# Performance work log

Measured on AMD Instinct MI355X. Metric: run time of the kernel, lower is better.

The kernel has to match this reference:

```python
import jax, jax.numpy as jnp
import numpy as np

B, N, C_IN, C_MID, H, N_CLS = 128, 2048, 3, 64, 128, 40
EPS = 1e-5

def setup_inputs() -> dict:
    key = jax.random.key(0)
    ks = jax.random.split(key, 12)
    sc = lambda fan: 1.0 / np.sqrt(fan)
    return {
        "x": jax.random.normal(ks[0], (B, N, C_IN), jnp.float32),
        "conv_w": jax.random.normal(ks[1], (C_MID, C_IN), jnp.float32) * sc(C_IN),
        "conv_b": jnp.zeros((C_MID,), jnp.float32),
        "gamma": jnp.ones((C_MID,), jnp.float32),
        "beta": jnp.zeros((C_MID,), jnp.float32),
        "running_mean": jax.random.normal(ks[2], (C_MID,), jnp.float32) * 0.1,
        "running_var": jax.random.uniform(ks[3], (C_MID,), jnp.float32) + 0.5,
        "W_ih": jax.random.normal(ks[4], (4 * H, C_MID), jnp.float32) * sc(H),
        "W_hh": jax.random.normal(ks[5], (4 * H, H), jnp.float32) * sc(H),
        "b_ih": jax.random.normal(ks[6], (4 * H,), jnp.float32) * sc(H),
        "b_hh": jax.random.normal(ks[7], (4 * H,), jnp.float32) * sc(H),
        "W_out": jax.random.normal(ks[8], (N_CLS, H), jnp.float32) * sc(H),
        "b_out": jnp.zeros((N_CLS,), jnp.float32),
    }

def reference(x, conv_w, conv_b, gamma, beta, running_mean, running_var,
              W_ih, W_hh, b_ih, b_hh, W_out, b_out):
    # Conv1d(3,64,1) == per-point linear; BN (inference form) + ReLU.  [B,N,64]
    h = jnp.einsum('bnc,oc->bno', x, conv_w) + conv_b
    inv = gamma * jax.lax.rsqrt(running_var + EPS)
    h = jax.nn.relu((h - running_mean) * inv + beta)
    # Precompute input-side gate projections for all timesteps: [B,N,4H]
    xg = jnp.einsum('bnc,gc->bng', h, W_ih) + b_ih + b_hh
    Whh_T = W_hh.T  # [H,4H]

    def step(carry, xg_t):
        h_prev, c_prev = carry
        g = xg_t + h_prev @ Whh_T  # [B,4H]
        i, f, gg, o = jnp.split(g, 4, axis=-1)  # PyTorch gate order i,f,g,o
        i = jax.nn.sigmoid(i)
        f = jax.nn.sigmoid(f)
        gg = jnp.tanh(gg)
        o = jax.nn.sigmoid(o)
        c = f * c_prev + i * gg
        h_new = o * jnp.tanh(c)
        return (h_new, c), None

    init = (jnp.zeros((x.shape[0], W_hh.shape[1]), x.dtype),
            jnp.zeros((x.shape[0], W_hh.shape[1]), x.dtype))
    (h_last, _), _ = jax.lax.scan(step, init, jnp.swapaxes(xg, 0, 1))
    # Only the last timestep feeds the classifier head.
    return h_last @ W_out.T + b_out
```

## Files before the change

### kernel.cpp

```cpp
#include <hip/hip_runtime.h>
#include <math.h>

#define BB 128
#define NN 2048
#define CMID 64
#define HH 128
#define NCLS 40
#define CHUNK 128
#define EPSV 1e-5f

#define HCP 80
#define HP  36

__device__ __forceinline__ float fsigmoid(float x) {
    return 1.0f / (1.0f + __expf(-x));
}
__device__ __forceinline__ float ftanh2(float x) {
    return 2.0f / (1.0f + __expf(-2.0f * x)) - 1.0f;
}
__device__ __forceinline__ void fma4(float& a, const float4 w, const float4 v) {
    a = fmaf(w.x, v.x, a);
    a = fmaf(w.y, v.y, a);
    a = fmaf(w.z, v.z, a);
    a = fmaf(w.w, v.w, a);
}

__global__ __attribute__((amdgpu_flat_work_group_size(512, 512),
                          amdgpu_waves_per_eu(2, 2)))
void lstm_seq_kernel(const float* __restrict__ x,
                     const float* __restrict__ conv_w, const float* __restrict__ conv_b,
                     const float* __restrict__ gamma,  const float* __restrict__ beta,
                     const float* __restrict__ rmean,  const float* __restrict__ rvar,
                     const float* __restrict__ W_ih,   const float* __restrict__ W_hh,
                     const float* __restrict__ b_ih,   const float* __restrict__ b_hh,
                     const float* __restrict__ W_out,  const float* __restrict__ b_out,
                     float* __restrict__ out)
{
    __shared__ float hc_s[CHUNK * HCP];
    __shared__ float h_s[2][4 * HP];
    __shared__ float cA0[CMID], cA1[CMID], cA2[CMID], cD[CMID];

    const int t = threadIdx.x;
    const int b = blockIdx.x;
    const int j = t >> 2;
    const int s = t & 3;

    if (t < CMID) {
        float inv = gamma[t] * rsqrtf(rvar[t] + EPSV);
        cA0[t] = conv_w[t * 3 + 0] * inv;
        cA1[t] = conv_w[t * 3 + 1] * inv;
        cA2[t] = conv_w[t * 3 + 2] * inv;
        cD[t]  = (conv_b[t] - rmean[t]) * inv + beta[t];
    }
    if (t < 2 * 4 * HP) ((float*)h_s)[t] = 0.0f;

    float4 wih[4][4];
    float4 whh[4][8];
    float  bias[4];
    #pragma unroll
    for (int g = 0; g < 4; ++g) {
        const int r = g * HH + j;
        const float* pih = W_ih + (size_t)r * CMID + s * 16;
        #pragma unroll
        for (int i = 0; i < 4; ++i) wih[g][i] = *(const float4*)(pih + 4 * i);
        const float* phh = W_hh + (size_t)r * HH + s * 32;
        #pragma unroll
        for (int i = 0; i < 8; ++i) whh[g][i] = *(const float4*)(phh + 4 * i);
        bias[g] = b_ih[r] + b_hh[r];
    }

    float c_reg = 0.0f;
    const float* xb = x + (size_t)b * NN * 3;

    for (int ch = 0; ch < NN / CHUNK; ++ch) {
        const int base = ch * CHUNK;
        __syncthreads();

        #pragma unroll
        for (int i = 0; i < (CHUNK * CMID) / 512; ++i) {
            int v  = i * 512 + t;
            int n  = v >> 6;
            int cc = v & 63;
            float x0 = xb[(base + n) * 3 + 0];
            float x1 = xb[(base + n) * 3 + 1];
            float x2 = xb[(base + n) * 3 + 2];
            float hcv = fmaxf(cD[cc] + cA0[cc] * x0 + cA1[cc] * x1 + cA2[cc] * x2, 0.0f);
            hc_s[n * HCP + (cc >> 4) * 20 + (cc & 15)] = hcv;
        }
        __syncthreads();

        for (int k = 0; k < CHUNK; ++k) {
            const int p = (base + k) & 1;
            float a0 = 0.f, a1 = 0.f, a2 = 0.f, a3 = 0.f;

            const float4* hcp = (const float4*)&hc_s[k * HCP + s * 20];
            const float4* hp  = (const float4*)&h_s[p][s * HP];

            #pragma unroll
            for (int i = 0; i < 4; ++i) {
                float4 v = hcp[i];
                fma4(a0, wih[0][i], v); fma4(a1, wih[1][i], v);
                fma4(a2, wih[2][i], v); fma4(a3, wih[3][i], v);
            }
            #pragma unroll
            for (int i = 0; i < 8; ++i) {
                float4 u = hp[i];
                fma4(a0, whh[0][i], u); fma4(a1, whh[1][i], u);
                fma4(a2, whh[2][i], u); fma4(a3, whh[3][i], u);
            }

            #pragma unroll
            for (int m = 1; m <= 2; m <<= 1) {
                a0 += __shfl_xor(a0, m);
                a1 += __shfl_xor(a1, m);
                a2 += __shfl_xor(a2, m);
                a3 += __shfl_xor(a3, m);
            }

            float gi = fsigmoid(a0 + bias[0]);
            float gf = fsigmoid(a1 + bias[1]);
            float gg = ftanh2(a2 + bias[2]);
            float go = fsigmoid(a3 + bias[3]);
            c_reg = gf * c_reg + gi * gg;
            float hv = go * ftanh2(c_reg);

            if (s == 0) h_s[p ^ 1][(j >> 5) * HP + (j & 31)] = hv;
            __syncthreads();
        }
    }

    if (t < NCLS) {
        float acc = b_out[t];
        const float* wr = W_out + (size_t)t * HH;
        #pragma unroll
        for (int jj = 0; jj < HH; ++jj)
            acc = fmaf(wr[jj], h_s[0][(jj >> 5) * HP + (jj & 31)], acc);
        out[(size_t)b * NCLS + t] = acc;
    }
}

extern "C" void kernel_launch(void* const* d_in, const int* in_sizes, int n_in,
                              void* d_out, int out_size, void* d_ws, size_t ws_size,
                              hipStream_t stream) {
    const float* x      = (const float*)d_in[0];
    const float* conv_w = (const float*)d_in[1];
    const float* conv_b = (const float*)d_in[2];
    const float* gamma  = (const float*)d_in[3];
    const float* beta   = (const float*)d_in[4];
    const float* rmean  = (const float*)d_in[5];
    const float* rvar   = (const float*)d_in[6];
    const float* W_ih   = (const float*)d_in[7];
    const float* W_hh   = (const float*)d_in[8];
    const float* b_ih   = (const float*)d_in[9];
    const float* b_hh   = (const float*)d_in[10];
    const float* W_out  = (const float*)d_in[11];
    const float* b_out  = (const float*)d_in[12];
    float* out = (float*)d_out;

    lstm_seq_kernel<<<BB, 512, 0, stream>>>(x, conv_w, conv_b, gamma, beta,
                                            rmean, rvar, W_ih, W_hh, b_ih, b_hh,
                                            W_out, b_out, out);
}
```

Before: 1.927 ms.

## Split each LSTM row pair across 8 lanes with reshaped shared-memory layouts

Changes the work split so each group of 8 lanes handles two hidden units (j and j+64) over 8-wide input slices, in place of one unit over 4-wide slices. Shared buffers are relaid out (unpadded hc_s, h_p[2][8][20]), the reduction uses three shuffle stages, and weight preloads go through inline-asm loads that wait after each one. The aim is to reduce shared-memory read traffic per lane and give more independent FMA chains per step. In exchange the timestep loop carries more shuffles and duplicated activation math, and the unpadded hc_s layout may cause bank conflicts.

```diff
diff --git a/kernel.cpp b/kernel.cpp
--- a/kernel.cpp
+++ b/kernel.cpp
@@ -8,9 +8,6 @@
 #define NCLS 40
 #define CHUNK 128
 #define EPSV 1e-5f
-
-#define HCP 80
-#define HP  36
 
 __device__ __forceinline__ float fsigmoid(float x) {
     return 1.0f / (1.0f + __expf(-x));
@@ -24,6 +21,18 @@
     a = fmaf(w.z, v.z, a);
     a = fmaf(w.w, v.w, a);
 }
+__device__ __forceinline__ float4 pin_load4(const float* p) {
+    float4 r;
+    asm volatile("global_load_dwordx4 %0, %1, off\n\ts_waitcnt vmcnt(0)"
+                 : "=v"(r) : "v"(p) : "memory");
+    return r;
+}
+__device__ __forceinline__ float pin_load1(const float* p) {
+    float r;
+    asm volatile("global_load_dword %0, %1, off\n\ts_waitcnt vmcnt(0)"
+                 : "=v"(r) : "v"(p) : "memory");
+    return r;
+}
 
 __global__ __attribute__((amdgpu_flat_work_group_size(512, 512),
                           amdgpu_waves_per_eu(2, 2)))
@@ -36,14 +45,14 @@
                      const float* __restrict__ W_out,  const float* __restrict__ b_out,
                      float* __restrict__ out)
 {
-    __shared__ float hc_s[CHUNK * HCP];
-    __shared__ float h_s[2][4 * HP];
+    __shared__ float hc_s[CHUNK * CMID];
+    __shared__ float h_p[2][8][20];
     __shared__ float cA0[CMID], cA1[CMID], cA2[CMID], cD[CMID];
 
     const int t = threadIdx.x;
     const int b = blockIdx.x;
-    const int j = t >> 2;
-    const int s = t & 3;
+    const int g = t >> 3;
+    const int s = t & 7;
 
     if (t < CMID) {
         float inv = gamma[t] * rsqrtf(rvar[t] + EPSV);
@@ -52,24 +61,27 @@
         cA2[t] = conv_w[t * 3 + 2] * inv;
         cD[t]  = (conv_b[t] - rmean[t]) * inv + beta[t];
     }
-    if (t < 2 * 4 * HP) ((float*)h_s)[t] = 0.0f;
+    if (t < 2 * 8 * 20) ((float*)h_p)[t] = 0.0f;
 
-    float4 wih[4][4];
-    float4 whh[4][8];
-    float  bias[4];
+    float4 wih[4][2][2];
+    float4 whh[4][2][4];
+    float  bias[4][2];
     #pragma unroll
-    for (int g = 0; g < 4; ++g) {
-        const int r = g * HH + j;
-        const float* pih = W_ih + (size_t)r * CMID + s * 16;
+    for (int q = 0; q < 4; ++q) {
         #pragma unroll
-        for (int i = 0; i < 4; ++i) wih[g][i] = *(const float4*)(pih + 4 * i);
-        const float* phh = W_hh + (size_t)r * HH + s * 32;
-        #pragma unroll
-        for (int i = 0; i < 8; ++i) whh[g][i] = *(const float4*)(phh + 4 * i);
-        bias[g] = b_ih[r] + b_hh[r];
+        for (int u = 0; u < 2; ++u) {
+            const int r = q * HH + g + u * 64;
+            const float* pih = W_ih + (size_t)r * CMID + s * 8;
+            wih[q][u][0] = pin_load4(pih);
+            wih[q][u][1] = pin_load4(pih + 4);
+            const float* phh = W_hh + (size_t)r * HH + s * 16;
+            #pragma unroll
+            for (int i = 0; i < 4; ++i) whh[q][u][i] = pin_load4(phh + 4 * i);
+            bias[q][u] = pin_load1(b_ih + r) + pin_load1(b_hh + r);
+        }
     }
 
-    float c_reg = 0.0f;
+    float c0 = 0.0f, c1 = 0.0f;
     const float* xb = x + (size_t)b * NN * 3;
 
     for (int ch = 0; ch < NN / CHUNK; ++ch) {
@@ -85,46 +97,62 @@
             float x1 = xb[(base + n) * 3 + 1];
             float x2 = xb[(base + n) * 3 + 2];
             float hcv = fmaxf(cD[cc] + cA0[cc] * x0 + cA1[cc] * x1 + cA2[cc] * x2, 0.0f);
-            hc_s[n * HCP + (cc >> 4) * 20 + (cc & 15)] = hcv;
+            hc_s[n * CMID + cc] = hcv;
         }
         __syncthreads();
 
+        #pragma unroll 2
         for (int k = 0; k < CHUNK; ++k) {
-            const int p = (base + k) & 1;
-            float a0 = 0.f, a1 = 0.f, a2 = 0.f, a3 = 0.f;
+            const int p = k & 1;
+            float a[4][2] = {{0.f, 0.f}, {0.f, 0.f}, {0.f, 0.f}, {0.f, 0.f}};
 
-            const float4* hcp = (const float4*)&hc_s[k * HCP + s * 20];
-            const float4* hp  = (const float4*)&h_s[p][s * HP];
+            const float4* hcp = (const float4*)&hc_s[k * CMID + s * 8];
+            const float4* hp  = (const float4*)&h_p[p][s][0];
 
+            float4 v0 = hcp[0], v1 = hcp[1];
+            #pragma unroll
+            for (int q = 0; q < 4; ++q) {
+                fma4(a[q][0], wih[q][0][0], v0); fma4(a[q][1], wih[q][1][0], v0);
+                fma4(a[q][0], wih[q][0][1], v1); fma4(a[q][1], wih[q][1][1], v1);
+            }
             #pragma unroll
             for (int i = 0; i < 4; ++i) {
-                float4 v = hcp[i];
-                fma4(a0, wih[0][i], v); fma4(a1, wih[1][i], v);
-                fma4(a2, wih[2][i], v); fma4(a3, wih[3][i], v);
-            }
-            #pragma unroll
-            for (int i = 0; i < 8; ++i) {
-                float4 u = hp[i];
-                fma4(a0, whh[0][i], u); fma4(a1, whh[1][i], u);
-                fma4(a2, whh[2][i], u); fma4(a3, whh[3][i], u);
+                float4 uv = hp[i];
+                #pragma unroll
+                for (int q = 0; q < 4; ++q) {
+                    fma4(a[q][0], whh[q][0][i], uv);
+                    fma4(a[q][1], whh[q][1][i], uv);
+                }
             }
 
             #pragma unroll
-            for (int m = 1; m <= 2; m <<= 1) {
-                a0 += __shfl_xor(a0, m);
-                a1 += __shfl_xor(a1, m);
-                a2 += __shfl_xor(a2, m);
-                a3 += __shfl_xor(a3, m);
+            for (int m = 1; m <= 4; m <<= 1) {
+                #pragma unroll
+                for (int q = 0; q < 4; ++q) {
+                    a[q][0] += __shfl_xor(a[q][0], m);
+                    a[q][1] += __shfl_xor(a[q][1], m);
+                }
             }
 
-            float gi = fsigmoid(a0 + bias[0]);
-            float gf = fsigmoid(a1 + bias[1]);
-            float gg = ftanh2(a2 + bias[2]);
-            float go = fsigmoid(a3 + bias[3]);
-            c_reg = gf * c_reg + gi * gg;
-            float hv = go * ftanh2(c_reg);
+            float gi0 = fsigmoid(a[0][0] + bias[0][0]);
+            float gf0 = fsigmoid(a[1][0] + bias[1][0]);
+            float gg0 = ftanh2 (a[2][0] + bias[2][0]);
+            float go0 = fsigmoid(a[3][0] + bias[3][0]);
+            float gi1 = fsigmoid(a[0][1] + bias[0][1]);
+            float gf1 = fsigmoid(a[1][1] + bias[1][1]);
+            float gg1 = ftanh2 (a[2][1] + bias[2][1]);
+            float go1 = fsigmoid(a[3][1] + bias[3][1]);
 
-            if (s == 0) h_s[p ^ 1][(j >> 5) * HP + (j & 31)] = hv;
+            c0 = gf0 * c0 + gi0 * gg0;
+            c1 = gf1 * c1 + gi1 * gg1;
+            float hv0 = go0 * ftanh2(c0);
+            float hv1 = go1 * ftanh2(c1);
+
+            if (s == 0) {
+                const int j1 = g + 64;
+                h_p[p ^ 1][g >> 4][g & 15]   = hv0;
+                h_p[p ^ 1][j1 >> 4][j1 & 15] = hv1;
+            }
             __syncthreads();
         }
     }
@@ -134,7 +162,7 @@
         const float* wr = W_out + (size_t)t * HH;
         #pragma unroll
         for (int jj = 0; jj < HH; ++jj)
-            acc = fmaf(wr[jj], h_s[0][(jj >> 5) * HP + (jj & 31)], acc);
+            acc = fmaf(wr[jj], h_p[0][jj >> 4][jj & 15], acc);
         out[(size_t)b * NCLS + t] = acc;
     }
 }
```

After: 3.058 ms. 1.59x slower.

## Precompute input gate projections per chunk into LDS before the recurrent loop

Applied to the files above, without the earlier changes.

Each chunk's input-side gate projections (W_ih times conv features plus bias) are now computed as a register-tiled batched matmul into shared memory. This takes the W_ih multiply off the serial per-timestep critical path, so each step only does the W_hh matvec plus a read of the precomputed gates. It also frees the W_ih registers and changes the launch bounds. In exchange, W_ih is reloaded from global/L2 for every chunk, the chunk size is halved, and more LDS is used.

```diff
diff --git a/kernel.cpp b/kernel.cpp
--- a/kernel.cpp
+++ b/kernel.cpp
@@ -5,12 +5,11 @@
 #define NN 2048
 #define CMID 64
 #define HH 128
+#define G4 512
 #define NCLS 40
-#define CHUNK 128
+#define CH 64
+#define NCH (NN / CH)
 #define EPSV 1e-5f
-
-#define HCP 80
-#define HP  36
 
 __device__ __forceinline__ float fsigmoid(float x) {
     return 1.0f / (1.0f + __expf(-x));
@@ -25,8 +24,7 @@
     a = fmaf(w.w, v.w, a);
 }
 
-__global__ __attribute__((amdgpu_flat_work_group_size(512, 512),
-                          amdgpu_waves_per_eu(2, 2)))
+__global__ __launch_bounds__(512, 1)
 void lstm_seq_kernel(const float* __restrict__ x,
                      const float* __restrict__ conv_w, const float* __restrict__ conv_b,
                      const float* __restrict__ gamma,  const float* __restrict__ beta,
@@ -36,9 +34,11 @@
                      const float* __restrict__ W_out,  const float* __restrict__ b_out,
                      float* __restrict__ out)
 {
-    __shared__ float hc_s[CHUNK * HCP];
-    __shared__ float h_s[2][4 * HP];
-    __shared__ float cA0[CMID], cA1[CMID], cA2[CMID], cD[CMID];
+    __shared__ float xg_s[CH][G4];
+    __shared__ float hcT[CMID][CH];
+    __shared__ float h_p[2][4][36];
+    __shared__ float bias_s[G4];
+    __shared__ float cf[4][CMID];
 
     const int t = threadIdx.x;
     const int b = blockIdx.x;
@@ -47,84 +47,119 @@
 
     if (t < CMID) {
         float inv = gamma[t] * rsqrtf(rvar[t] + EPSV);
-        cA0[t] = conv_w[t * 3 + 0] * inv;
-        cA1[t] = conv_w[t * 3 + 1] * inv;
-        cA2[t] = conv_w[t * 3 + 2] * inv;
-        cD[t]  = (conv_b[t] - rmean[t]) * inv + beta[t];
+        cf[0][t] = conv_w[t * 3 + 0] * inv;
+        cf[1][t] = conv_w[t * 3 + 1] * inv;
+        cf[2][t] = conv_w[t * 3 + 2] * inv;
+        cf[3][t] = (conv_b[t] - rmean[t]) * inv + beta[t];
     }
-    if (t < 2 * 4 * HP) ((float*)h_s)[t] = 0.0f;
+    bias_s[t] = b_ih[t] + b_hh[t];
+    if (t < 2 * 4 * 36) ((float*)h_p)[t] = 0.0f;
 
-    float4 wih[4][4];
     float4 whh[4][8];
-    float  bias[4];
     #pragma unroll
-    for (int g = 0; g < 4; ++g) {
-        const int r = g * HH + j;
-        const float* pih = W_ih + (size_t)r * CMID + s * 16;
+    for (int q = 0; q < 4; ++q) {
+        const float* p = W_hh + (size_t)(q * HH + j) * HH + s * 32;
         #pragma unroll
-        for (int i = 0; i < 4; ++i) wih[g][i] = *(const float4*)(pih + 4 * i);
-        const float* phh = W_hh + (size_t)r * HH + s * 32;
-        #pragma unroll
-        for (int i = 0; i < 8; ++i) whh[g][i] = *(const float4*)(phh + 4 * i);
-        bias[g] = b_ih[r] + b_hh[r];
+        for (int i = 0; i < 8; ++i) whh[q][i] = *(const float4*)(p + 4 * i);
     }
 
     float c_reg = 0.0f;
     const float* xb = x + (size_t)b * NN * 3;
 
-    for (int ch = 0; ch < NN / CHUNK; ++ch) {
-        const int base = ch * CHUNK;
+    for (int ch = 0; ch < NCH; ++ch) {
+        const int base = ch * CH;
         __syncthreads();
 
-        #pragma unroll
-        for (int i = 0; i < (CHUNK * CMID) / 512; ++i) {
-            int v  = i * 512 + t;
-            int n  = v >> 6;
-            int cc = v & 63;
+        {
+            const int n = t & 63;
+            const int c0 = t >> 6;
             float x0 = xb[(base + n) * 3 + 0];
             float x1 = xb[(base + n) * 3 + 1];
             float x2 = xb[(base + n) * 3 + 2];
-            float hcv = fmaxf(cD[cc] + cA0[cc] * x0 + cA1[cc] * x1 + cA2[cc] * x2, 0.0f);
-            hc_s[n * HCP + (cc >> 4) * 20 + (cc & 15)] = hcv;
+            #pragma unroll
+            for (int i = 0; i < 8; ++i) {
+                int c = i * 8 + c0;
+                float hv = cf[3][c] + cf[0][c] * x0 + cf[1][c] * x1 + cf[2][c] * x2;
+                hcT[c][n] = fmaxf(hv, 0.0f);
+            }
         }
         __syncthreads();
 
-        for (int k = 0; k < CHUNK; ++k) {
-            const int p = (base + k) & 1;
-            float a0 = 0.f, a1 = 0.f, a2 = 0.f, a3 = 0.f;
-
-            const float4* hcp = (const float4*)&hc_s[k * HCP + s * 20];
-            const float4* hp  = (const float4*)&h_s[p][s * HP];
-
+        for (int pass = 0; pass < 2; ++pass) {
+            const int r0 = (pass * 2 + 0) * HH + j;
+            const int r1 = (pass * 2 + 1) * HH + j;
+            float acc0[16], acc1[16];
+            const float b0 = bias_s[r0], b1 = bias_s[r1];
             #pragma unroll
-            for (int i = 0; i < 4; ++i) {
-                float4 v = hcp[i];
-                fma4(a0, wih[0][i], v); fma4(a1, wih[1][i], v);
-                fma4(a2, wih[2][i], v); fma4(a3, wih[3][i], v);
+            for (int n = 0; n < 16; ++n) { acc0[n] = b0; acc1[n] = b1; }
+            const float* w0p = W_ih + (size_t)r0 * CMID;
+            const float* w1p = W_ih + (size_t)r1 * CMID;
+            for (int k4 = 0; k4 < 16; ++k4) {
+                float4 w0 = *(const float4*)(w0p + k4 * 4);
+                float4 w1 = *(const float4*)(w1p + k4 * 4);
+                const float* w0f = (const float*)&w0;
+                const float* w1f = (const float*)&w1;
+                #pragma unroll
+                for (int kk = 0; kk < 4; ++kk) {
+                    const int k = k4 * 4 + kk;
+                    const float wa = w0f[kk];
+                    const float wb = w1f[kk];
+                    const float4* hc4 = (const float4*)&hcT[k][s * 16];
+                    #pragma unroll
+                    for (int i2 = 0; i2 < 4; ++i2) {
+                        float4 hv = hc4[i2];
+                        acc0[i2 * 4 + 0] = fmaf(wa, hv.x, acc0[i2 * 4 + 0]);
+                        acc0[i2 * 4 + 1] = fmaf(wa, hv.y, acc0[i2 * 4 + 1]);
+                        acc0[i2 * 4 + 2] = fmaf(wa, hv.z, acc0[i2 * 4 + 2]);
+                        acc0[i2 * 4 + 3] = fmaf(wa, hv.w, acc0[i2 * 4 + 3]);
+                        acc1[i2 * 4 + 0] = fmaf(wb, hv.x, acc1[i2 * 4 + 0]);
+                        acc1[i2 * 4 + 1] = fmaf(wb, hv.y, acc1[i2 * 4 + 1]);
+                        acc1[i2 * 4 + 2] = fmaf(wb, hv.z, acc1[i2 * 4 + 2]);
+                        acc1[i2 * 4 + 3] = fmaf(wb, hv.w, acc1[i2 * 4 + 3]);
+                    }
+                }
             }
             #pragma unroll
+            for (int n = 0; n < 16; ++n) {
+                xg_s[s * 16 + n][r0] = acc0[n];
+                xg_s[s * 16 + n][r1] = acc1[n];
+            }
+        }
+        __syncthreads();
+
+        for (int k = 0; k < CH; ++k) {
+            const int p = (base + k) & 1;
+            float a0, a1, a2, a3;
+            if (s == 0) {
+                a0 = xg_s[k][0 * HH + j];
+                a1 = xg_s[k][1 * HH + j];
+                a2 = xg_s[k][2 * HH + j];
+                a3 = xg_s[k][3 * HH + j];
+            } else {
+                a0 = a1 = a2 = a3 = 0.0f;
+            }
+            const float4* hp = (const float4*)&h_p[p][s][0];
+            #pragma unroll
             for (int i = 0; i < 8; ++i) {
-                float4 u = hp[i];
-                fma4(a0, whh[0][i], u); fma4(a1, whh[1][i], u);
-                fma4(a2, whh[2][i], u); fma4(a3, whh[3][i], u);
+                float4 hv = hp[i];
+                fma4(a0, whh[0][i], hv);
+                fma4(a1, whh[1][i], hv);
+                fma4(a2, whh[2][i], hv);
+                fma4(a3, whh[3][i], hv);
             }
+            a0 += __shfl_xor(a0, 1); a0 += __shfl_xor(a0, 2);
+            a1 += __shfl_xor(a1, 1); a1 += __shfl_xor(a1, 2);
+            a2 += __shfl_xor(a2, 1); a2 += __shfl_xor(a2, 2);
+            a3 += __shfl_xor(a3, 1); a3 += __shfl_xor(a3, 2);
 
-            #pragma unroll
-            for (int m = 1; m <= 2; m <<= 1) {
-                a0 += __shfl_xor(a0, m);
-                a1 += __shfl_xor(a1, m);
-                a2 += __shfl_xor(a2, m);
-                a3 += __shfl_xor(a3, m);
-            }
-
-            float gi = fsigmoid(a0 + bias[0]);
-            float gf = fsigmoid(a1 + bias[1]);
-            float gg = ftanh2(a2 + bias[2]);
-            float go = fsigmoid(a3 + bias[3]);
+            float gi = fsigmoid(a0);
+            float gf = fsigmoid(a1);
+            float gg = ftanh2(a2);
+            float go = fsigmoid(a3);
             c_reg = gf * c_reg + gi * gg;
             float hv = go * ftanh2(c_reg);
 
-            if (s == 0) h_s[p ^ 1][(j >> 5) * HP + (j & 31)] = hv;
+            if (s == 0) h_p[p ^ 1][j >> 5][j & 31] = hv;
             __syncthreads();
         }
     }
@@ -134,7 +169,7 @@
         const float* wr = W_out + (size_t)t * HH;
         #pragma unroll
         for (int jj = 0; jj < HH; ++jj)
-            acc = fmaf(wr[jj], h_s[0][(jj >> 5) * HP + (jj & 31)], acc);
+            acc = fmaf(wr[jj], h_p[0][jj >> 5][jj & 31], acc);
         out[(size_t)b * NCLS + t] = acc;
     }
 }
@@ -156,6 +191,7 @@
     const float* W_out  = (const float*)d_in[11];
     const float* b_out  = (const float*)d_in[12];
     float* out = (float*)d_out;
+    (void)d_ws; (void)ws_size; (void)in_sizes; (void)n_in; (void)out_size;
 
     lstm_seq_kernel<<<BB, 512, 0, stream>>>(x, conv_w, conv_b, gamma, beta,
                                             rmean, rvar, W_ih, W_hh, b_ih, b_hh,
```

Result: slower. 2.137 ms (+10.9%).
